# Performance work log

Measured on AMD Instinct MI355X. Metric: run time of the kernel, lower is better.

Reference implementation:

```python
import jax, jax.numpy as jnp
import numpy as np

NUM_HEADS = 16
NUM_GROUPS = 4
EPS = 1e-6


def _rope_tables(seq_len, head_dim):
    inv_freq = 1.0 / (10000.0 ** (jnp.arange(0, head_dim, 2, dtype=jnp.float32) / head_dim))
    t = jnp.arange(seq_len, dtype=jnp.float32)
    freqs = jnp.outer(t, inv_freq)  # [s, hd//2]
    return jnp.sin(freqs), jnp.cos(freqs)


def _apply_rope(x, sin, cos):
    # x: [b, s, h, hd]; sin/cos: [s, hd//2] -> broadcast over batch and heads
    sin = sin[None, :, None, :]
    cos = cos[None, :, None, :]
    x1 = x[..., ::2]
    x2 = x[..., 1::2]
    out1 = x1 * cos - x2 * sin
    out2 = x1 * sin + x2 * cos
    return jnp.stack([out1, out2], axis=-1).reshape(x.shape).astype(x.dtype)


def _rmsnorm(x, scale):
    var = jnp.mean(jnp.square(x), axis=-1, keepdims=True)
    return x * jax.lax.rsqrt(var + EPS) * scale


def setup_inputs() -> dict:
    key = jax.random.key(0)
    b, s, d = 16, 512, 2048
    hd = d // NUM_HEADS
    g = NUM_GROUPS
    ks = jax.random.split(key, 9)
    std = 0.02
    return {
        "x": jax.random.normal(ks[0], (b, s, d), dtype=jnp.float32),
        "Wq": jax.random.normal(ks[1], (d, d), dtype=jnp.float32) * std,
        "bq": jnp.zeros((d,), dtype=jnp.float32),
        "Wk": jax.random.normal(ks[2], (d, g * hd), dtype=jnp.float32) * std,
        "bk": jnp.zeros((g * hd,), dtype=jnp.float32),
        "Wv": jax.random.normal(ks[3], (d, g * hd), dtype=jnp.float32) * std,
        "bv": jnp.zeros((g * hd,), dtype=jnp.float32),
        "Wo": jax.random.normal(ks[4], (d, d), dtype=jnp.float32) * std,
        "bo": jnp.zeros((d,), dtype=jnp.float32),
        "q_norm_scale": jnp.ones((hd,), dtype=jnp.float32),
        "k_norm_scale": jnp.ones((hd,), dtype=jnp.float32),
    }


def reference(x, Wq, bq, Wk, bk, Wv, bv, Wo, bo, q_norm_scale, k_norm_scale):
    b, s, d = x.shape
    H, G = NUM_HEADS, NUM_GROUPS
    hd = d // H
    P = H // G  # queries per kv group
    inv_sqrt_hd = hd ** (-0.5)

    q = (x @ Wq + bq).reshape(b, s, H, hd)
    k = (x @ Wk + bk).reshape(b, s, G, hd)
    v = (x @ Wv + bv).reshape(b, s, G, hd)

    q = _rmsnorm(q, q_norm_scale)
    k = _rmsnorm(k, k_norm_scale)

    sin, cos = _rope_tables(s, hd)
    q = _apply_rope(q, sin, cos) * inv_sqrt_hd  # module pre-scales q
    k = _apply_rope(k, sin, cos)

    # GQA attention with causal mask; dot_product_attention applies an
    # additional 1/sqrt(hd) scale on top of the module's pre-scaling.
    qg = q.reshape(b, s, G, P, hd)
    logits = jnp.einsum("bsgph,btgh->bgpst", qg, k) * inv_sqrt_hd
    causal = jnp.tril(jnp.ones((s, s), dtype=bool))
    logits = jnp.where(causal[None, None, None, :, :], logits, jnp.finfo(logits.dtype).min)
    attn = jax.nn.softmax(logits, axis=-1)
    out = jnp.einsum("bgpst,btgh->bsgph", attn, v).reshape(b, s, d)
    return out @ Wo + bo
```

## Files before the change

kernel.cpp:

```cpp
#include <hip/hip_runtime.h>
#include <stdint.h>

typedef __attribute__((ext_vector_type(4))) float floatx4;
typedef __attribute__((ext_vector_type(16))) float floatx16;
typedef __attribute__((ext_vector_type(8))) short short8;

#define BB 16
#define SS 512
#define DD 2048
#define HH_ 16
#define HD 128
#define GG 4
#define MM (BB*SS)
#define NQKV 3072

__device__ __forceinline__ unsigned short f2bf(float f){
  unsigned u = __builtin_bit_cast(unsigned, f);
  u += 0x7fffu + ((u >> 16) & 1u);
  return (unsigned short)(u >> 16);
}
__device__ __forceinline__ float bf2f_lo(unsigned d){
  return __builtin_bit_cast(float, d << 16);
}
__device__ __forceinline__ float bf2f_hi(unsigned d){
  return __builtin_bit_cast(float, d & 0xffff0000u);
}

__device__ __forceinline__ void async_copy16(const void* g, void* l){
  __builtin_amdgcn_global_load_lds((const __attribute__((address_space(1))) unsigned*)g,
                                   (__attribute__((address_space(3))) unsigned*)l,
                                   16, 0, 0);
}

#define PB_CVT   16384
#define PB_TRQ   (PB_CVT + 4096)
#define PB_TRK   (PB_TRQ + 1024)
#define PB_TRV   (PB_TRK + 1024)
#define PB_TRO   (PB_TRV + 4096)
#define PB_ALL   (PB_TRO + 12)

__global__ __launch_bounds__(256) void prep_kernel(
    const float* __restrict__ x,
    const float* __restrict__ Wq, const float* __restrict__ Wk,
    const float* __restrict__ Wv, const float* __restrict__ Wo,
    const float* __restrict__ bq, const float* __restrict__ bk,
    const float* __restrict__ bv,
    unsigned short* __restrict__ xb, unsigned short* __restrict__ WqkvT,
    unsigned short* __restrict__ WoT, float* __restrict__ bqkv)
{
  __shared__ float tile[32][33];
  const int bid = blockIdx.x, tid = threadIdx.x;

  if (bid < PB_CVT) {
    const int i = bid * 256 + tid;
    float4 f = ((const float4*)x)[i];
    ushort4 o;
    o.x = f2bf(f.x); o.y = f2bf(f.y); o.z = f2bf(f.z); o.w = f2bf(f.w);
    ((ushort4*)xb)[i] = o;
    return;
  }
  if (bid < PB_TRO) {
    const float* src; unsigned short* dst; int R, C, b2;
    if (bid < PB_TRQ)      { src = Wq; dst = WqkvT;                          R = 2048; C = 2048; b2 = bid - PB_CVT; }
    else if (bid < PB_TRK) { src = Wk; dst = WqkvT + (size_t)2048 * 2048;    R = 2048; C = 512;  b2 = bid - PB_TRQ; }
    else if (bid < PB_TRV) { src = Wv; dst = WqkvT + (size_t)2560 * 2048;    R = 2048; C = 512;  b2 = bid - PB_TRK; }
    else                   { src = Wo; dst = WoT;                            R = 2048; C = 2048; b2 = bid - PB_TRV; }
    const int nbx = C >> 5;
    const int c0 = (b2 % nbx) * 32, r0 = (b2 / nbx) * 32;
    const int tx = tid & 31, ty = tid >> 5;
    #pragma unroll
    for (int j = 0; j < 32; j += 8)
      tile[ty + j][tx] = src[(size_t)(r0 + ty + j) * C + (c0 + tx)];
    __syncthreads();
    #pragma unroll
    for (int j = 0; j < 32; j += 8)
      dst[(size_t)(c0 + ty + j) * R + (r0 + tx)] = f2bf(tile[tx][ty + j]);
    return;
  }
  {
    const int i = (bid - PB_TRO) * 256 + tid;
    if (i < NQKV)
      bqkv[i] = (i < 2048) ? bq[i] : (i < 2560 ? bk[i - 2048] : bv[i - 2560]);
  }
}

template<bool OUT_BF16>
__global__ __launch_bounds__(512, 2) void gemm256_kernel(
    const unsigned short* __restrict__ A,
    const unsigned short* __restrict__ Bt,
    void* __restrict__ Cout,
    const float* __restrict__ bias,
    int N, int K, int ldc)
{
  __shared__ unsigned short sA[4 * 128 * 64];
  __shared__ unsigned short sB[4 * 128 * 64];

  const int tid  = threadIdx.x;
  const int wave = tid >> 6, lane = tid & 63;
  const int wm = wave >> 2, wn = wave & 3;
  const int l15 = lane & 15, l7 = lane & 7, q4 = lane >> 4;

  const int nbn = N >> 8;
  const int cpx = gridDim.x >> 3;
  const int bid = (blockIdx.x & 7) * cpx + (blockIdx.x >> 3);
  const int m0 = (bid / nbn) * 256;
  const int n0 = (bid % nbn) * 256;

  const int rowOff = wave * 8 + (lane >> 3);
  const int glog   = l7 ^ ((lane >> 3) & 7);
  const unsigned short* gA = A  + (size_t)(m0 + rowOff) * K + glog * 8;
  const unsigned short* gB = Bt + (size_t)(n0 + rowOff) * K + glog * 8;

#define STAGE_A(j, tt) do { \
    unsigned short* d_ = &sA[(2 * ((tt) & 1) + (j)) * 8192 + wave * 512]; \
    const unsigned short* s_ = gA + (size_t)((j) * 128) * K + (tt) * 64; \
    async_copy16(s_, d_); \
    async_copy16(s_ + (size_t)64 * K, d_ + 4096); } while (0)
#define STAGE_B(j, tt) do { \
    unsigned short* d_ = &sB[(2 * ((tt) & 1) + (j)) * 8192 + wave * 512]; \
    const unsigned short* s_ = gB + (size_t)((j) * 128) * K + (tt) * 64; \
    async_copy16(s_, d_); \
    async_copy16(s_ + (size_t)64 * K, d_ + 4096); } while (0)

  STAGE_B(0, 0); STAGE_B(1, 0); STAGE_A(0, 0); STAGE_A(1, 0);
  STAGE_B(0, 1); STAGE_B(1, 1); STAGE_A(0, 1);

  floatx4 acc[8][4];
  #pragma unroll
  for (int i = 0; i < 8; ++i)
    #pragma unroll
    for (int j = 0; j < 4; ++j)
      acc[i][j] = (floatx4){0.f, 0.f, 0.f, 0.f};

  asm volatile("s_waitcnt vmcnt(6)" ::: "memory");
  __builtin_amdgcn_s_barrier();

  short8 aF[4][2], bF[4][2];
  const int NT = K >> 6;

  const unsigned short* pA = &sA[l15 * 64];
  const unsigned short* pB = &sB[((wn & 1) * 64 + l15) * 64];
  const int g0 = ((0 + q4) ^ l7) * 8;
  const int g1 = ((4 + q4) ^ l7) * 8;

#define LDA_(fa_, rb_, sa_) do { \
    aF[fa_][0] = *(const short8*)(pA + (sa_) * 8192 + ((rb_) + (fa_) * 16) * 64 + g0); \
    aF[fa_][1] = *(const short8*)(pA + (sa_) * 8192 + ((rb_) + (fa_) * 16) * 64 + g1); } while (0)
#define LDB_(fb_, sb_) do { \
    bF[fb_][0] = *(const short8*)(pB + (sb_) * 8192 + (fb_) * 16 * 64 + g0); \
    bF[fb_][1] = *(const short8*)(pB + (sb_) * 8192 + (fb_) * 16 * 64 + g1); } while (0)
#define MFMA_Q(fa0, fb0) \
    _Pragma("unroll") \
    for (int fa = 0; fa < 4; ++fa) { \
      _Pragma("unroll") \
      for (int fb = 0; fb < 2; ++fb) { \
        acc[(fa0)+fa][(fb0)+fb] = __builtin_amdgcn_mfma_f32_16x16x32_bf16(aF[fa][0], bF[(fb0)+fb][0], acc[(fa0)+fa][(fb0)+fb], 0, 0, 0); \
        acc[(fa0)+fa][(fb0)+fb] = __builtin_amdgcn_mfma_f32_16x16x32_bf16(aF[fa][1], bF[(fb0)+fb][1], acc[(fa0)+fa][(fb0)+fb], 0, 0, 0); \
      } \
    }

  #pragma unroll 1
  for (int t = 0; t < NT; ++t) {
    const int sa = 2 * (t & 1) + wm;
    const int sb = 2 * (t & 1) + (wn >> 1);
    LDA_(0, 0, sa); LDA_(1, 0, sa); LDA_(2, 0, sa); LDA_(3, 0, sa);
    LDB_(0, sb); LDB_(1, sb);
    if (t + 1 < NT) STAGE_A(1, t + 1);
    __builtin_amdgcn_s_barrier();
    asm volatile("s_waitcnt lgkmcnt(0)" ::: "memory");
    __builtin_amdgcn_sched_barrier(0);
    __builtin_amdgcn_s_setprio(1);
    MFMA_Q(0, 0);
    __builtin_amdgcn_s_setprio(0);
    __builtin_amdgcn_s_barrier();
    LDB_(2, sb); LDB_(3, sb);
    if (t + 2 < NT) STAGE_B(0, t + 2);
    __builtin_amdgcn_s_barrier();
    asm volatile("s_waitcnt lgkmcnt(0)" ::: "memory");
    __builtin_amdgcn_sched_barrier(0);
    __builtin_amdgcn_s_setprio(1);
    MFMA_Q(0, 2);
    __builtin_amdgcn_s_setprio(0);
    __builtin_amdgcn_s_barrier();
    LDA_(0, 64, sa); LDA_(1, 64, sa); LDA_(2, 64, sa); LDA_(3, 64, sa);
    if (t + 2 < NT) STAGE_B(1, t + 2);
    __builtin_amdgcn_s_barrier();
    asm volatile("s_waitcnt lgkmcnt(0)" ::: "memory");
    __builtin_amdgcn_sched_barrier(0);
    __builtin_amdgcn_s_setprio(1);
    MFMA_Q(4, 0);
    __builtin_amdgcn_s_setprio(0);
    __builtin_amdgcn_s_barrier();
    if (t + 2 < NT) {
      STAGE_A(0, t + 2);
      asm volatile("s_waitcnt vmcnt(6)" ::: "memory");
    } else if (t + 1 < NT) {
      asm volatile("s_waitcnt vmcnt(0)" ::: "memory");
    }
    __builtin_amdgcn_s_barrier();
    __builtin_amdgcn_s_setprio(1);
    MFMA_Q(4, 2);
    __builtin_amdgcn_s_setprio(0);
    __builtin_amdgcn_s_barrier();
  }
#undef STAGE_A
#undef STAGE_B
#undef LDA_
#undef LDB_
#undef MFMA_Q

  const int r4 = q4 * 4;
  #pragma unroll
  for (int fb = 0; fb < 4; ++fb) {
    const int col = n0 + wn * 64 + fb * 16 + l15;
    const float bval = bias[col];
    #pragma unroll
    for (int fa = 0; fa < 8; ++fa) {
      const size_t rowb = (size_t)(m0 + wm * 128 + fa * 16 + r4);
      #pragma unroll
      for (int r = 0; r < 4; ++r) {
        const float v = acc[fa][fb][r] + bval;
        if (OUT_BF16)
          ((unsigned short*)Cout)[(rowb + r) * ldc + col] = f2bf(v);
        else
          ((float*)Cout)[(rowb + r) * ldc + col] = v;
      }
    }
  }
}

__global__ __launch_bounds__(256) void norm_vtr_kernel(
    unsigned short* __restrict__ qkv,
    const float* __restrict__ qs, const float* __restrict__ ks,
    unsigned short* __restrict__ vt)
{
  __shared__ unsigned short tileV[32][34];
  const int bid = blockIdx.x, tid = threadIdx.x;

  if (bid < 40960) {
    const int wave = tid >> 6, lane = tid & 63;
    const int gw  = bid * 4 + wave;
    const int row = gw / 20;
    const int hh  = gw % 20;
    const bool isq = hh < 16;

    unsigned* p = (unsigned*)(qkv + (size_t)row * NQKV + hh * 128) + lane;
    unsigned d = *p;
    float x1 = bf2f_lo(d), x2 = bf2f_hi(d);

    float ss = x1 * x1 + x2 * x2;
    #pragma unroll
    for (int off = 32; off; off >>= 1) ss += __shfl_xor(ss, off, 64);
    const float r = rsqrtf(ss * (1.f / 128.f) + 1e-6f);

    const float2 sc = ((const float2*)(isq ? qs : ks))[lane];
    float n1 = x1 * r * sc.x;
    float n2 = x2 * r * sc.y;

    const float t = (float)(row & (SS - 1));
    const float freq = __expf((float)lane * (-2.f / 128.f) * 9.21034037197618f);
    float sn, cs;
    __sincosf(t * freq, &sn, &cs);
    float o1 = n1 * cs - n2 * sn;
    float o2 = n1 * sn + n2 * cs;
    if (isq) { o1 *= (1.f / 128.f); o2 *= (1.f / 128.f); }

    *p = (unsigned)f2bf(o1) | ((unsigned)f2bf(o2) << 16);
    return;
  }
  {
    const int b2 = bid - 40960;
    const int hd0 = (b2 & 3) * 32, t0 = ((b2 >> 2) & 15) * 32, bg = b2 >> 6;
    const int tx = tid & 31, ty = tid >> 5;
    const int b = bg >> 2, g = bg & 3;
    const unsigned short* src = qkv + (size_t)b * SS * NQKV + 2560 + g * HD;
    #pragma unroll
    for (int j = 0; j < 32; j += 8)
      tileV[ty + j][tx] = src[(size_t)(t0 + ty + j) * NQKV + hd0 + tx];
    __syncthreads();
    unsigned short* dst = vt + (size_t)bg * HD * SS;
    #pragma unroll
    for (int j = 0; j < 32; j += 8)
      dst[(size_t)(hd0 + ty + j) * SS + t0 + tx] = tileV[tx][ty + j];
  }
}

__global__ __launch_bounds__(256, 4) void fattn_kernel(
    const unsigned short* __restrict__ qkv,
    const unsigned short* __restrict__ vtb,
    unsigned short* __restrict__ aout)
{
  __shared__ unsigned short sK[64 * 128];
  __shared__ unsigned short sV[128 * 64];
  __shared__ unsigned short sP[4][16 * 64];

  const int lane = threadIdx.x & 63, wave = threadIdx.x >> 6;
  const int quad = lane >> 4, col = lane & 15;
  const int idx = blockIdx.x;
  const int qb = 7 - (idx >> 8);
  const int bh = idx & 255;
  const int b = bh >> 4, h = bh & 15, g = h >> 2;

  const int qrow = qb * 64 + wave * 16 + col;
  const unsigned short* qg = qkv + ((size_t)(b * SS + qrow)) * NQKV + h * HD + quad * 8;
  short8 qf[4];
  #pragma unroll
  for (int c = 0; c < 4; ++c) qf[c] = *(const short8*)(qg + c * 32);

  const unsigned short* kg = qkv + (size_t)b * SS * NQKV + 2048 + g * HD;
  const unsigned short* vg = vtb + ((size_t)(b * GG + g)) * HD * SS;

  floatx4 acc_o[8];
  #pragma unroll
  for (int i = 0; i < 8; ++i) acc_o[i] = (floatx4){0.f, 0.f, 0.f, 0.f};
  float m[4] = {-INFINITY, -INFINITY, -INFINITY, -INFINITY};
  float l[4] = {0.f, 0.f, 0.f, 0.f};

  for (int kt = 0; kt <= qb; ++kt) {
    const int t0 = kt * 64;
    #pragma unroll
    for (int c = 0; c < 4; ++c) {
      const int ci = c * 4 + wave;
      { const int r  = ci * 4 + (lane >> 4);
        const int gl = (lane & 15) ^ (r & 15);
        async_copy16(kg + (size_t)(t0 + r) * NQKV + gl * 8, &sK[ci * 512]); }
      { const int r  = ci * 8 + (lane >> 3);
        const int gl = (lane & 7) ^ (r & 7);
        async_copy16(vg + (size_t)r * SS + t0 + gl * 8, &sV[ci * 512]); }
    }
    __syncthreads();

    floatx4 sc[4];
    #pragma unroll
    for (int s = 0; s < 4; ++s) sc[s] = (floatx4){0.f, 0.f, 0.f, 0.f};
    #pragma unroll
    for (int s = 0; s < 4; ++s) {
      const int trow = s * 16 + col;
      #pragma unroll
      for (int c = 0; c < 4; ++c) {
        const int p = (c * 4 + quad) ^ (trow & 15);
        const short8 kf = *(const short8*)(&sK[trow * 128 + p * 8]);
        sc[s] = __builtin_amdgcn_mfma_f32_16x16x32_bf16(qf[c], kf, sc[s], 0, 0, 0);
      }
    }

    if (kt == qb) {
      #pragma unroll
      for (int s = 0; s < 4; ++s)
        #pragma unroll
        for (int r = 0; r < 4; ++r)
          if (s * 16 + col > wave * 16 + quad * 4 + r) sc[s][r] = -1e30f;
    }

    float mx[4], alpha[4], lsum[4];
    #pragma unroll
    for (int r = 0; r < 4; ++r) {
      mx[r] = fmaxf(fmaxf(sc[0][r], sc[1][r]), fmaxf(sc[2][r], sc[3][r]));
      #pragma unroll
      for (int off = 8; off; off >>= 1) mx[r] = fmaxf(mx[r], __shfl_xor(mx[r], off, 16));
      mx[r] = fmaxf(mx[r], m[r]);
      alpha[r] = __expf(m[r] - mx[r]);
      m[r] = mx[r];
      lsum[r] = 0.f;
    }
    #pragma unroll
    for (int s = 0; s < 4; ++s)
      #pragma unroll
      for (int r = 0; r < 4; ++r) {
        const float p = __expf(sc[s][r] - m[r]);
        lsum[r] += p;
        const int row = quad * 4 + r;
        const int slot = (s * 2 + (col >> 3)) ^ (row & 7);
        sP[wave][row * 64 + slot * 8 + (col & 7)] = f2bf(p);
      }
    #pragma unroll
    for (int r = 0; r < 4; ++r) {
      #pragma unroll
      for (int off = 8; off; off >>= 1) lsum[r] += __shfl_xor(lsum[r], off, 16);
      l[r] = l[r] * alpha[r] + lsum[r];
    }
    #pragma unroll
    for (int n = 0; n < 8; ++n)
      #pragma unroll
      for (int r = 0; r < 4; ++r) acc_o[n][r] *= alpha[r];

    __asm__ volatile("s_waitcnt lgkmcnt(0)" ::: "memory");

    short8 pf[2];
    #pragma unroll
    for (int kc = 0; kc < 2; ++kc)
      pf[kc] = *(const short8*)(&sP[wave][col * 64 + ((kc * 4 + quad) ^ (col & 7)) * 8]);
    #pragma unroll
    for (int n = 0; n < 8; ++n) {
      const int hdrow = n * 16 + col;
      #pragma unroll
      for (int kc = 0; kc < 2; ++kc) {
        const int p = (kc * 4 + quad) ^ (hdrow & 7);
        const short8 vf = *(const short8*)(&sV[hdrow * 64 + p * 8]);
        acc_o[n] = __builtin_amdgcn_mfma_f32_16x16x32_bf16(pf[kc], vf, acc_o[n], 0, 0, 0);
      }
    }
    __syncthreads();
  }

  float inv[4];
  #pragma unroll
  for (int r = 0; r < 4; ++r) inv[r] = 1.f / l[r];
  unsigned short* ob = aout + ((size_t)(b * SS + qb * 64 + wave * 16)) * DD + h * HD;
  #pragma unroll
  for (int n = 0; n < 8; ++n)
    #pragma unroll
    for (int r = 0; r < 4; ++r)
      ob[(size_t)(quad * 4 + r) * DD + n * 16 + col] = f2bf(acc_o[n][r] * inv[r]);
}

extern "C" void kernel_launch(void* const* d_in, const int* in_sizes, int n_in,
                              void* d_out, int out_size, void* d_ws, size_t ws_size,
                              hipStream_t stream) {
  const float* x   = (const float*)d_in[0];
  const float* Wq  = (const float*)d_in[1];
  const float* bq  = (const float*)d_in[2];
  const float* Wk  = (const float*)d_in[3];
  const float* bk  = (const float*)d_in[4];
  const float* Wv  = (const float*)d_in[5];
  const float* bv  = (const float*)d_in[6];
  const float* Wo  = (const float*)d_in[7];
  const float* bo  = (const float*)d_in[8];
  const float* qns = (const float*)d_in[9];
  const float* kns = (const float*)d_in[10];

  char* ws = (char*)d_ws;
  unsigned short* xb    = (unsigned short*)(ws);
  unsigned short* vtb   = (unsigned short*)(ws);
  unsigned short* WqkvT = (unsigned short*)(ws + 33554432);
  unsigned short* WoT   = (unsigned short*)(ws + 46137344);
  float*          bqkv  = (float*)         (ws + 54525952);
  unsigned short* qkv   = (unsigned short*)(ws + 54538240);
  unsigned short* aout  = (unsigned short*)(ws + 104869888);

  prep_kernel<<<PB_ALL, 256, 0, stream>>>(x, Wq, Wk, Wv, Wo, bq, bk, bv,
                                          xb, WqkvT, WoT, bqkv);
  gemm256_kernel<true><<<384, 512, 0, stream>>>(xb, WqkvT, qkv, bqkv,
                                                NQKV, DD, NQKV);
  norm_vtr_kernel<<<45056, 256, 0, stream>>>(qkv, qns, kns, vtb);
  fattn_kernel<<<2048, 256, 0, stream>>>(qkv, vtb, aout);
  gemm256_kernel<false><<<256, 512, 0, stream>>>(aout, WoT, d_out, bo,
                                                 DD, DD, DD);
  (void)in_sizes; (void)n_in; (void)out_size; (void)ws_size;
}
```

Before: 436.3 us.

## Restructure GEMM main loop to prefetch full tiles two steps ahead with fewer barriers

The bf16 GEMM main loop now issues both halves of each A and B tile for step t+2 together, instead of splitting A staging between t+1 and t+2. The prologue therefore preloads a full second stage and waits on vmcnt(8) rather than vmcnt(6). Per-iteration barriers drop from eight to four, and the explicit lgkmcnt waits and sched_barriers are removed, leaving the compiler to place the LDS waits and interleave loads with MFMAs. The risks are longer stalls on the larger global-load groups and a weaker instruction ordering than the hand-placed schedule. An unused zero vector is also added.

```diff
diff --git a/kernel.cpp b/kernel.cpp
--- a/kernel.cpp
+++ b/kernel.cpp
@@ -121,19 +121,23 @@
     const unsigned short* s_ = gB + (size_t)((j) * 128) * K + (tt) * 64; \
     async_copy16(s_, d_); \
     async_copy16(s_ + (size_t)64 * K, d_ + 4096); } while (0)
+#define FENCE() asm volatile("" ::: "memory")
+#define BAR()   do { FENCE(); __builtin_amdgcn_s_barrier(); FENCE(); } while (0)
 
   STAGE_B(0, 0); STAGE_B(1, 0); STAGE_A(0, 0); STAGE_A(1, 0);
-  STAGE_B(0, 1); STAGE_B(1, 1); STAGE_A(0, 1);
-
+  STAGE_B(0, 1); STAGE_B(1, 1); STAGE_A(0, 1); STAGE_A(1, 1);
+
+  floatx16 zero16 = {0.f};
   floatx4 acc[8][4];
   #pragma unroll
   for (int i = 0; i < 8; ++i)
     #pragma unroll
     for (int j = 0; j < 4; ++j)
       acc[i][j] = (floatx4){0.f, 0.f, 0.f, 0.f};
-
-  asm volatile("s_waitcnt vmcnt(6)" ::: "memory");
-  __builtin_amdgcn_s_barrier();
+  (void)zero16;
+
+  asm volatile("s_waitcnt vmcnt(8)" ::: "memory");
+  BAR();
 
   short8 aF[4][2], bF[4][2];
   const int NT = K >> 6;
@@ -163,51 +167,41 @@
   for (int t = 0; t < NT; ++t) {
     const int sa = 2 * (t & 1) + wm;
     const int sb = 2 * (t & 1) + (wn >> 1);
+    LDB_(0, sb); LDB_(1, sb);
     LDA_(0, 0, sa); LDA_(1, 0, sa); LDA_(2, 0, sa); LDA_(3, 0, sa);
-    LDB_(0, sb); LDB_(1, sb);
-    if (t + 1 < NT) STAGE_A(1, t + 1);
-    __builtin_amdgcn_s_barrier();
-    asm volatile("s_waitcnt lgkmcnt(0)" ::: "memory");
-    __builtin_amdgcn_sched_barrier(0);
     __builtin_amdgcn_s_setprio(1);
     MFMA_Q(0, 0);
     __builtin_amdgcn_s_setprio(0);
-    __builtin_amdgcn_s_barrier();
+    BAR();
     LDB_(2, sb); LDB_(3, sb);
-    if (t + 2 < NT) STAGE_B(0, t + 2);
-    __builtin_amdgcn_s_barrier();
-    asm volatile("s_waitcnt lgkmcnt(0)" ::: "memory");
-    __builtin_amdgcn_sched_barrier(0);
     __builtin_amdgcn_s_setprio(1);
     MFMA_Q(0, 2);
     __builtin_amdgcn_s_setprio(0);
-    __builtin_amdgcn_s_barrier();
+    BAR();
     LDA_(0, 64, sa); LDA_(1, 64, sa); LDA_(2, 64, sa); LDA_(3, 64, sa);
-    if (t + 2 < NT) STAGE_B(1, t + 2);
-    __builtin_amdgcn_s_barrier();
-    asm volatile("s_waitcnt lgkmcnt(0)" ::: "memory");
-    __builtin_amdgcn_sched_barrier(0);
+    if (t + 2 < NT) { STAGE_B(0, t + 2); STAGE_B(1, t + 2); }
     __builtin_amdgcn_s_setprio(1);
     MFMA_Q(4, 0);
     __builtin_amdgcn_s_setprio(0);
-    __builtin_amdgcn_s_barrier();
+    BAR();
     if (t + 2 < NT) {
-      STAGE_A(0, t + 2);
-      asm volatile("s_waitcnt vmcnt(6)" ::: "memory");
+      STAGE_A(0, t + 2); STAGE_A(1, t + 2);
+      asm volatile("s_waitcnt vmcnt(8)" ::: "memory");
     } else if (t + 1 < NT) {
       asm volatile("s_waitcnt vmcnt(0)" ::: "memory");
     }
-    __builtin_amdgcn_s_barrier();
     __builtin_amdgcn_s_setprio(1);
     MFMA_Q(4, 2);
     __builtin_amdgcn_s_setprio(0);
-    __builtin_amdgcn_s_barrier();
+    BAR();
   }
 #undef STAGE_A
 #undef STAGE_B
 #undef LDA_
 #undef LDB_
 #undef MFMA_Q
+#undef FENCE
+#undef BAR
 
   const int r4 = q4 * 4;
   #pragma unroll
```

Result: faster. 426.0 us (-2.4%).
